# Performance work log

Measured on AMD Instinct MI355X. Metric: run time of the kernel, lower is better.

The kernel has to match this reference:

```python
import jax, jax.numpy as jnp
import numpy as np

SEQ = 4096
EMBED = 1280
HEADS = 16
HEAD_DIM = EMBED // HEADS  # 80


def rotate_half(x):
    # interleaved rotate: out[..., 2i] = -x[..., 2i+1]; out[..., 2i+1] = x[..., 2i]
    x_even = x[..., ::2]
    x_odd = x[..., 1::2]
    return jnp.stack((-x_odd, x_even), axis=-1).reshape(x.shape)


def setup_inputs() -> dict:
    key = jax.random.key(0)
    ks = jax.random.split(key, 7)
    return {
        "hidden_states": jax.random.normal(ks[0], (SEQ, EMBED), dtype=jnp.float32),
        "cos": jax.random.uniform(ks[1], (SEQ, HEAD_DIM), dtype=jnp.float32),
        "sin": jax.random.uniform(ks[2], (SEQ, HEAD_DIM), dtype=jnp.float32),
        "w_qkv": jax.random.normal(ks[3], (EMBED, 3 * EMBED), dtype=jnp.float32) * 0.02,
        "b_qkv": jax.random.normal(ks[4], (3 * EMBED,), dtype=jnp.float32) * 0.02,
        "w_proj": jax.random.normal(ks[5], (EMBED, EMBED), dtype=jnp.float32) * 0.02,
        "b_proj": jax.random.normal(ks[6], (EMBED,), dtype=jnp.float32) * 0.02,
    }


def reference(hidden_states, cos, sin, w_qkv, b_qkv, w_proj, b_proj):
    S = hidden_states.shape[0]
    # QKV projection: (S, 3E) -> (S, 3, H, D)
    qkv = (hidden_states @ w_qkv + b_qkv).reshape(S, 3, HEADS, HEAD_DIM)
    q, k, v = qkv[:, 0], qkv[:, 1], qkv[:, 2]  # each (S, H, D)

    # RoPE in float32, cos/sin broadcast over heads: (S, 1, D)
    dt = q.dtype
    qf, kf = q.astype(jnp.float32), k.astype(jnp.float32)
    c = cos[:, None, :].astype(jnp.float32)
    s = sin[:, None, :].astype(jnp.float32)
    q = (qf * c + rotate_half(qf) * s).astype(dt)
    k = (kf * c + rotate_half(kf) * s).astype(dt)

    scaling = HEAD_DIM ** -0.5
    # attention scores per head: (H, S, S)
    scores = jnp.einsum("shd,thd->hst", q, k) * scaling
    attn = jax.nn.softmax(scores.astype(jnp.float32), axis=-1).astype(dt)
    # weighted values: (S, H, D)
    out = jnp.einsum("hst,thd->shd", attn, v).reshape(S, EMBED)
    return out @ w_proj + b_proj
```

## Files before the change

### kernel.cpp

```cpp
#include <hip/hip_runtime.h>
#include <hip/hip_bf16.h>

#define SEQ   4096
#define EMBED 1280
#define NH    16
#define HD    80
#define K1    EMBED
#define N1    (3*EMBED)

typedef short bfrag_t __attribute__((ext_vector_type(8)));
typedef float f32x4   __attribute__((ext_vector_type(4)));
typedef float f32x16  __attribute__((ext_vector_type(16)));

static __device__ __forceinline__ unsigned short f2bf(float x){
    __hip_bfloat16 h = __float2bfloat16(x);
    return __builtin_bit_cast(unsigned short, h);
}
static __device__ __forceinline__ float bf2f(unsigned short u){
    unsigned int v = ((unsigned int)u) << 16;
    return __builtin_bit_cast(float, v);
}

static __device__ __forceinline__ unsigned int pack2bf(float a, float b){
    unsigned int ua = __builtin_bit_cast(unsigned int, a) + 0x8000u;
    unsigned int ub = __builtin_bit_cast(unsigned int, b) + 0x8000u;
#if __has_builtin(__builtin_amdgcn_perm)
    return __builtin_amdgcn_perm(ub, ua, 0x07060302u);
#else
    return (ua >> 16) | (ub & 0xFFFF0000u);
#endif
}

static __device__ __forceinline__ float fast_exp2(float x){
#if __has_builtin(__builtin_amdgcn_exp2f)
    return __builtin_amdgcn_exp2f(x);
#else
    return __expf(x * 0.69314718056f);
#endif
}

static __device__ __forceinline__ void gload_lds16(const void* g, void* l){
#if __has_builtin(__builtin_amdgcn_global_load_lds)
    __builtin_amdgcn_global_load_lds(
        (const __attribute__((address_space(1))) unsigned int*)g,
        (__attribute__((address_space(3))) unsigned int*)l, 16, 0, 0);
#else
    *(uint4*)l = *(const uint4*)g;
#endif
}

static __device__ __forceinline__ bfrag_t ld_frag8(const unsigned short* p){
    uint2 lo = *(const uint2*)p;
    uint2 hi = *(const uint2*)(p + 4);
    uint4 u; u.x = lo.x; u.y = lo.y; u.z = hi.x; u.w = hi.y;
    return __builtin_bit_cast(bfrag_t, u);
}

#define CONV_BLOCKS (SEQ*EMBED/4/256)
#define TQ_BX (N1/32)
#define TQ_BLOCKS (TQ_BX*(K1/32))
#define TP_BX (EMBED/32)
#define TP_BLOCKS (TP_BX*(EMBED/32))

__global__ __launch_bounds__(256)
void prep_all(const float* __restrict__ hs, unsigned short* __restrict__ hb,
              const float* __restrict__ wqkv, unsigned short* __restrict__ wqT,
              const float* __restrict__ wproj, unsigned short* __restrict__ wpT)
{
    __shared__ float t[32][33];
    int b = blockIdx.x;
    if (b < CONV_BLOCKS){
        int i = b * 256 + threadIdx.x;
        float4 v = ((const float4*)hs)[i];
        ushort4 r;
        r.x = f2bf(v.x); r.y = f2bf(v.y); r.z = f2bf(v.z); r.w = f2bf(v.w);
        ((ushort4*)hb)[i] = r;
        return;
    }
    const float* in; unsigned short* outp; int R, C, bc, br;
    if (b < CONV_BLOCKS + TQ_BLOCKS){
        b -= CONV_BLOCKS;
        in = wqkv; outp = wqT; R = K1; C = N1;
        bc = (b % TQ_BX) * 32; br = (b / TQ_BX) * 32;
    } else {
        b -= CONV_BLOCKS + TQ_BLOCKS;
        in = wproj; outp = wpT; R = EMBED; C = EMBED;
        bc = (b % TP_BX) * 32; br = (b / TP_BX) * 32;
    }
    int tx = threadIdx.x & 31, ty = threadIdx.x >> 5;
    for (int i = ty; i < 32; i += 8) t[i][tx] = in[(size_t)(br + i) * C + bc + tx];
    __syncthreads();
    for (int i = ty; i < 32; i += 8) outp[(size_t)(bc + i) * R + br + tx] = f2bf(t[tx][i]);
}


__global__ __launch_bounds__(256, 4)
void gemm_qkv(const unsigned short* __restrict__ A,
              const unsigned short* __restrict__ BT,
              const float* __restrict__ bias,
              const float* __restrict__ cosp, const float* __restrict__ sinp,
              unsigned short* __restrict__ qout, unsigned short* __restrict__ kout,
              unsigned short* __restrict__ vout,
              int M, int N, int K)
{
    __shared__ union {
        struct { unsigned short A[128*32]; unsigned short B[128*32]; } ab;
        unsigned short tr[4][64][72];
    } lds;

    int tid  = threadIdx.x;
    int lane = tid & 63, wave = tid >> 6;
    int wm = wave >> 1, wn = wave & 1;
    int quad = lane >> 4, l16 = lane & 15;
    int m0 = blockIdx.y * 128, n0 = blockIdx.x * 128;

    f32x4 acc[4][4] = {};
    const unsigned short* ga = A  + (size_t)(m0 + (tid>>2)) * K + (tid&3)*8;
    const unsigned short* gb = BT + (size_t)(n0 + (tid>>2)) * K + (tid&3)*8;

    for (int k0 = 0; k0 < K; k0 += 32){
        __syncthreads();
        gload_lds16(ga,                &lds.ab.A[tid*8]);
        gload_lds16(ga + (size_t)64*K, &lds.ab.A[2048 + tid*8]);
        gload_lds16(gb,                &lds.ab.B[tid*8]);
        gload_lds16(gb + (size_t)64*K, &lds.ab.B[2048 + tid*8]);
        ga += 32; gb += 32;
        __syncthreads();
        bfrag_t af[4], bf[4];
        #pragma unroll
        for (int i = 0; i < 4; i++)
            af[i] = *(const bfrag_t*)&lds.ab.A[(wm*64 + i*16 + l16)*32 + quad*8];
        #pragma unroll
        for (int j = 0; j < 4; j++)
            bf[j] = *(const bfrag_t*)&lds.ab.B[(wn*64 + j*16 + l16)*32 + quad*8];
        #pragma unroll
        for (int i = 0; i < 4; i++)
            #pragma unroll
            for (int j = 0; j < 4; j++)
                acc[i][j] = __builtin_amdgcn_mfma_f32_16x16x32_bf16(af[i], bf[j], acc[i][j], 0, 0, 0);
    }

    const float scaling = 0.11180339887498949f;

    if (n0 >= 2*EMBED){
        __syncthreads();
        #pragma unroll
        for (int j = 0; j < 4; j++){
            int colw = j*16 + l16;
            float b = bias[n0 + wn*64 + colw];
            #pragma unroll
            for (int i = 0; i < 4; i++){
                ushort4 u;
                u.x = f2bf(acc[i][j][0] + b);
                u.y = f2bf(acc[i][j][1] + b);
                u.z = f2bf(acc[i][j][2] + b);
                u.w = f2bf(acc[i][j][3] + b);
                *(ushort4*)&lds.tr[wave][colw][i*16 + quad*4] = u;
            }
        }
        int c8 = lane >> 3, rc = lane & 7;
        #pragma unroll
        for (int cg = 0; cg < 8; cg++){
            int colw = cg*8 + c8;
            size_t colg = (size_t)(n0 - 2*EMBED) + wn*64 + colw;
            int rowg = m0 + wm*64 + rc*8;
            *(uint4*)&vout[colg*SEQ + rowg] = *(const uint4*)&lds.tr[wave][colw][rc*8];
        }
        return;
    }

    #pragma unroll
    for (int i = 0; i < 4; i++)
    #pragma unroll
    for (int j = 0; j < 4; j++){
        int colj  = n0 + wn*64 + j*16;
        int which = colj / EMBED;
        int rem   = colj - which*EMBED;
        int hh    = rem / HD;
        int dd    = rem - hh*HD;
        float b = bias[colj + l16];
        unsigned short* dst = (which == 0) ? qout : kout;
        float mult = (which == 0) ? scaling : 1.f;
        #pragma unroll
        for (int r = 0; r < 4; r++){
            int row = m0 + wm*64 + i*16 + quad*4 + r;
            float v = acc[i][j][r] + b;
            float vo = __shfl_xor(v, 1, 64);
            float c = cosp[(size_t)row*HD + dd + l16];
            float s = sinp[(size_t)row*HD + dd + l16];
            float o = (l16 & 1) ? (v*c + vo*s) : (v*c - vo*s);
            dst[((size_t)hh*SEQ + row)*HD + dd + l16] = f2bf(o * mult);
        }
    }
}


__global__ __launch_bounds__(256, 4)
void gemm_proj(const unsigned short* __restrict__ A,
               const unsigned short* __restrict__ BT,
               const float* __restrict__ bias,
               float* __restrict__ out,
               int M, int N, int K)
{
    __shared__ unsigned short As[64*32];
    __shared__ unsigned short Bs[128*32];
    int tid  = threadIdx.x;
    int lane = tid & 63, wave = tid >> 6;
    int wm = wave & 1, wn = wave >> 1;
    int quad = lane >> 4, l16 = lane & 15;
    int m0 = blockIdx.y * 64, n0 = blockIdx.x * 128;

    f32x4 acc[2][4] = {};
    const unsigned short* ga = A  + (size_t)(m0 + (tid>>2)) * K + (tid&3)*8;
    const unsigned short* gb = BT + (size_t)(n0 + (tid>>2)) * K + (tid&3)*8;

    for (int k0 = 0; k0 < K; k0 += 32){
        __syncthreads();
        gload_lds16(ga,                &As[tid*8]);
        gload_lds16(gb,                &Bs[tid*8]);
        gload_lds16(gb + (size_t)64*K, &Bs[2048 + tid*8]);
        ga += 32; gb += 32;
        __syncthreads();
        bfrag_t af[2], bf[4];
        #pragma unroll
        for (int i = 0; i < 2; i++)
            af[i] = *(const bfrag_t*)&As[(wm*32 + i*16 + l16)*32 + quad*8];
        #pragma unroll
        for (int j = 0; j < 4; j++)
            bf[j] = *(const bfrag_t*)&Bs[(wn*64 + j*16 + l16)*32 + quad*8];
        #pragma unroll
        for (int i = 0; i < 2; i++)
            #pragma unroll
            for (int j = 0; j < 4; j++)
                acc[i][j] = __builtin_amdgcn_mfma_f32_16x16x32_bf16(af[i], bf[j], acc[i][j], 0, 0, 0);
    }

    #pragma unroll
    for (int i = 0; i < 2; i++)
    #pragma unroll
    for (int j = 0; j < 4; j++){
        int col = n0 + wn*64 + j*16 + l16;
        float b = bias[col];
        #pragma unroll
        for (int r = 0; r < 4; r++){
            int row = m0 + wm*32 + i*16 + quad*4 + r;
            out[(size_t)row * N + col] = acc[i][j][r] + b;
        }
    }
}


__global__ __launch_bounds__(256, 4)
void attn_mfma(const unsigned short* __restrict__ q,
               const unsigned short* __restrict__ k,
               const unsigned short* __restrict__ vt,
               unsigned short* __restrict__ out,
               unsigned short* __restrict__ opart,
               float* __restrict__ lpart,
               int iters)
{
    __shared__ unsigned short Vt[2][80*64];
    __shared__ unsigned short Ps[128][68];

    int tid  = threadIdx.x;
    int lane = tid & 63, wave = tid >> 6;
    int quad = lane >> 4, l16 = lane & 15;
    int l32  = lane & 31, h2 = lane >> 5;
    int h = blockIdx.y, q0 = blockIdx.x * 128;
    int split = blockIdx.z;
    int kb0 = split * iters * 64;
    int qrow = wave*32 + l32;

    const unsigned short* qh = q  + ((size_t)h*SEQ + q0)*HD;
    const unsigned short* kh = k  + (size_t)h*SEQ*HD;
    const unsigned short* vh = vt + (size_t)h*HD*SEQ;

    bfrag_t qf[5];
    #pragma unroll
    for (int kk = 0; kk < 5; kk++)
        qf[kk] = *(const bfrag_t*)&qh[(size_t)qrow*HD + (kk*2 + h2)*8];

    auto stage = [&](int buf, int kb){
        unsigned short* dst = &Vt[buf][0];
        #pragma unroll
        for (int rnd = 0; rnd < 3; rnd++){
            int idx = rnd*256 + tid;
            if (rnd < 2 || tid < 128){
                int row = idx >> 3, c = idx & 7;
                gload_lds16(&vh[(size_t)row*SEQ + kb + ((c ^ (row & 7)) << 3)], &dst[idx*8]);
            }
        }
    };

    stage(0, kb0);

    float la = 0.f, lb = 0.f;
    f32x4 o_[2][5] = {};

    const unsigned short* kp = kh + (size_t)(kb0 + l32)*HD + h2*8;
    const float LOG2E = 1.44269504f;
    const float BIAS2 = -17.3123405f;

    for (int kt = 0; kt < iters; kt++){
        f32x16 S0 = {}, S1 = {};
        #pragma unroll
        for (int kk = 0; kk < 5; kk++){
            bfrag_t kf0 = *(const bfrag_t*)(kp + kk*16);
            bfrag_t kf1 = *(const bfrag_t*)(kp + (size_t)32*HD + kk*16);
            S0 = __builtin_amdgcn_mfma_f32_32x32x16_bf16(kf0, qf[kk], S0, 0,0,0);
            S1 = __builtin_amdgcn_mfma_f32_32x32x16_bf16(kf1, qf[kk], S1, 0,0,0);
        }
        kp += (size_t)64*HD;

        #pragma unroll
        for (int r = 0; r < 16; r++){
            float p0 = fast_exp2(fmaf(S0[r], LOG2E, BIAS2));
            float p1 = fast_exp2(fmaf(S1[r], LOG2E, BIAS2));
            S0[r] = p0; S1[r] = p1;
            la += p0; lb += p1;
        }

        #pragma unroll
        for (int g = 0; g < 4; g++){
            uint2 w0, w1;
            w0.x = pack2bf(S0[g*4+0], S0[g*4+1]);
            w0.y = pack2bf(S0[g*4+2], S0[g*4+3]);
            w1.x = pack2bf(S1[g*4+0], S1[g*4+1]);
            w1.y = pack2bf(S1[g*4+2], S1[g*4+3]);
            *(uint2*)&Ps[qrow][g*8 + h2*4]      = w0;
            *(uint2*)&Ps[qrow][32 + g*8 + h2*4] = w1;
        }

        __syncthreads();
        if (kt + 1 < iters) stage((kt+1)&1, kb0 + (kt+1)*64);

        int buf = kt & 1;
        #pragma unroll
        for (int kk = 0; kk < 2; kk++){
            bfrag_t pf0 = ld_frag8(&Ps[wave*32      + l16][kk*32 + quad*8]);
            bfrag_t pf1 = ld_frag8(&Ps[wave*32 + 16 + l16][kk*32 + quad*8]);
            #pragma unroll
            for (int dt = 0; dt < 5; dt++){
                int row = dt*16 + l16;
                bfrag_t vf = *(const bfrag_t*)&Vt[buf][row*64 + (((kk*4+quad) ^ (l16 & 7)) << 3)];
                o_[0][dt] = __builtin_amdgcn_mfma_f32_16x16x32_bf16(vf, pf0, o_[0][dt], 0,0,0);
                o_[1][dt] = __builtin_amdgcn_mfma_f32_16x16x32_bf16(vf, pf1, o_[1][dt], 0,0,0);
            }
        }
    }

    float l_ = la + lb;
    l_ += __shfl_xor(l_, 32, 64);

    if (gridDim.z == 1){
        #pragma unroll
        for (int i = 0; i < 2; i++){
            float linv = 1.f / __shfl(l_, i*16 + l16, 64);
            int qg = q0 + wave*32 + i*16 + l16;
            #pragma unroll
            for (int dt = 0; dt < 5; dt++){
                int d = dt*16 + quad*4;
                ushort4 u;
                u.x = f2bf(o_[i][dt][0]*linv);
                u.y = f2bf(o_[i][dt][1]*linv);
                u.z = f2bf(o_[i][dt][2]*linv);
                u.w = f2bf(o_[i][dt][3]*linv);
                *(ushort4*)&out[(size_t)qg*EMBED + h*HD + d] = u;
            }
        }
    } else {
        if (h2 == 0)
            lpart[((size_t)(split*NH + h))*SEQ + q0 + qrow] = l_;
        #pragma unroll
        for (int i = 0; i < 2; i++){
            int qg = q0 + wave*32 + i*16 + l16;
            size_t base = (((size_t)(split*NH + h))*SEQ + qg)*HD;
            #pragma unroll
            for (int dt = 0; dt < 5; dt++){
                int d = dt*16 + quad*4;
                ushort4 u;
                u.x = f2bf(o_[i][dt][0]);
                u.y = f2bf(o_[i][dt][1]);
                u.z = f2bf(o_[i][dt][2]);
                u.w = f2bf(o_[i][dt][3]);
                *(ushort4*)&opart[base + d] = u;
            }
        }
    }
}

__global__ __launch_bounds__(256)
void attn_combine(const unsigned short* __restrict__ op,
                  const float* __restrict__ lp,
                  unsigned short* __restrict__ out,
                  int ns)
{
    int t = blockIdx.x*256 + threadIdx.x;
    int d8 = t % 10;
    int qh = t / 10;
    int q  = qh & (SEQ-1);
    int h  = qh >> 12;
    float lsum = 0.f;
    for (int s = 0; s < ns; s++) lsum += lp[((size_t)(s*NH + h))*SEQ + q];
    float inv = 1.f / lsum;
    float acc[8] = {};
    for (int s = 0; s < ns; s++){
        uint4 A = *(const uint4*)&op[(((size_t)(s*NH + h))*SEQ + q)*HD + d8*8];
        unsigned int* a = (unsigned int*)&A;
        #pragma unroll
        for (int e = 0; e < 4; e++){
            acc[2*e]   += bf2f((unsigned short)(a[e] & 0xffff));
            acc[2*e+1] += bf2f((unsigned short)(a[e] >> 16));
        }
    }
    uint4 R;
    unsigned int* r = (unsigned int*)&R;
    #pragma unroll
    for (int e = 0; e < 4; e++)
        r[e] = pack2bf(acc[2*e]*inv, acc[2*e+1]*inv);
    *(uint4*)&out[(size_t)q*EMBED + h*HD + d8*8] = R;
}


extern "C" void kernel_launch(void* const* d_in, const int* in_sizes, int n_in,
                              void* d_out, int out_size, void* d_ws, size_t ws_size,
                              hipStream_t stream)
{
    const float* hs    = (const float*)d_in[0];
    const float* cosp  = (const float*)d_in[1];
    const float* sinp  = (const float*)d_in[2];
    const float* wqkv  = (const float*)d_in[3];
    const float* bqkv  = (const float*)d_in[4];
    const float* wproj = (const float*)d_in[5];
    const float* bproj = (const float*)d_in[6];
    float* out = (float*)d_out;

    char* ws = (char*)d_ws;
    size_t off = 0;
    auto alloc = [&](size_t bytes){ void* p = ws + off; off += bytes; return p; };
    unsigned short* hb    = (unsigned short*)alloc((size_t)SEQ*EMBED*2);
    unsigned short* wqT   = (unsigned short*)alloc((size_t)N1*K1*2);
    unsigned short* wpT   = (unsigned short*)alloc((size_t)EMBED*EMBED*2);
    unsigned short* q_ws  = (unsigned short*)alloc((size_t)SEQ*EMBED*2);
    unsigned short* k_ws  = (unsigned short*)alloc((size_t)SEQ*EMBED*2);
    unsigned short* v_ws  = (unsigned short*)alloc((size_t)SEQ*EMBED*2);
    unsigned short* a_ws  = (unsigned short*)alloc((size_t)SEQ*EMBED*2);
    size_t base = off;
    size_t per_split = (size_t)NH*SEQ*HD*2 + (size_t)NH*SEQ*4;
    int nsplit = 1;
    if (ws_size >= base + 4*per_split)      nsplit = 4;
    else if (ws_size >= base + 2*per_split) nsplit = 2;
    unsigned short* opart = (unsigned short*)alloc((size_t)nsplit*NH*SEQ*HD*2);
    float*          lpart = (float*)alloc((size_t)nsplit*NH*SEQ*4);

    prep_all<<<CONV_BLOCKS + TQ_BLOCKS + TP_BLOCKS, 256, 0, stream>>>(
        hs, hb, wqkv, wqT, wproj, wpT);

    gemm_qkv<<<dim3(N1/128, SEQ/128), 256, 0, stream>>>(
        hb, wqT, bqkv, cosp, sinp, q_ws, k_ws, v_ws, SEQ, N1, K1);

    attn_mfma<<<dim3(SEQ/128, NH, nsplit), 256, 0, stream>>>(
        q_ws, k_ws, v_ws, a_ws, opart, lpart, (SEQ/64)/nsplit);
    if (nsplit > 1)
        attn_combine<<<NH*SEQ*10/256, 256, 0, stream>>>(opart, lpart, a_ws, nsplit);

    gemm_proj<<<dim3(EMBED/128, SEQ/64), 256, 0, stream>>>(
        a_ws, wpT, bproj, out, SEQ, EMBED, EMBED);
}
```

Baseline: 322.6 us.

## Split QK^T into two sequential halves, use hardware bf16 pack, cap split-K at two

```diff
diff --git a/kernel.cpp b/kernel.cpp
--- a/kernel.cpp
+++ b/kernel.cpp
@@ -22,12 +22,17 @@
 }
 
 static __device__ __forceinline__ unsigned int pack2bf(float a, float b){
+#if __has_builtin(__builtin_amdgcn_cvt_pk_bf16_f32)
+    short2 p = __builtin_amdgcn_cvt_pk_bf16_f32(a, b);
+    return __builtin_bit_cast(unsigned int, p);
+#else
     unsigned int ua = __builtin_bit_cast(unsigned int, a) + 0x8000u;
     unsigned int ub = __builtin_bit_cast(unsigned int, b) + 0x8000u;
 #if __has_builtin(__builtin_amdgcn_perm)
     return __builtin_amdgcn_perm(ub, ua, 0x07060302u);
 #else
     return (ua >> 16) | (ub & 0xFFFF0000u);
+#endif
 #endif
 }
 
@@ -302,33 +307,49 @@
     const float BIAS2 = -17.3123405f;
 
     for (int kt = 0; kt < iters; kt++){
-        f32x16 S0 = {}, S1 = {};
-        #pragma unroll
-        for (int kk = 0; kk < 5; kk++){
-            bfrag_t kf0 = *(const bfrag_t*)(kp + kk*16);
-            bfrag_t kf1 = *(const bfrag_t*)(kp + (size_t)32*HD + kk*16);
-            S0 = __builtin_amdgcn_mfma_f32_32x32x16_bf16(kf0, qf[kk], S0, 0,0,0);
-            S1 = __builtin_amdgcn_mfma_f32_32x32x16_bf16(kf1, qf[kk], S1, 0,0,0);
-        }
+        bfrag_t kf[5];
+        #pragma unroll
+        for (int kk = 0; kk < 5; kk++)
+            kf[kk] = *(const bfrag_t*)(kp + kk*16);
+        f32x16 S = {};
+        #pragma unroll
+        for (int kk = 0; kk < 5; kk++)
+            S = __builtin_amdgcn_mfma_f32_32x32x16_bf16(kf[kk], qf[kk], S, 0,0,0);
+
+        bfrag_t kg[5];
+        #pragma unroll
+        for (int kk = 0; kk < 5; kk++)
+            kg[kk] = *(const bfrag_t*)(kp + (size_t)32*HD + kk*16);
         kp += (size_t)64*HD;
 
         #pragma unroll
         for (int r = 0; r < 16; r++){
-            float p0 = fast_exp2(fmaf(S0[r], LOG2E, BIAS2));
-            float p1 = fast_exp2(fmaf(S1[r], LOG2E, BIAS2));
-            S0[r] = p0; S1[r] = p1;
-            la += p0; lb += p1;
-        }
-
+            float p = fast_exp2(fmaf(S[r], LOG2E, BIAS2));
+            S[r] = p; la += p;
+        }
         #pragma unroll
         for (int g = 0; g < 4; g++){
-            uint2 w0, w1;
-            w0.x = pack2bf(S0[g*4+0], S0[g*4+1]);
-            w0.y = pack2bf(S0[g*4+2], S0[g*4+3]);
-            w1.x = pack2bf(S1[g*4+0], S1[g*4+1]);
-            w1.y = pack2bf(S1[g*4+2], S1[g*4+3]);
-            *(uint2*)&Ps[qrow][g*8 + h2*4]      = w0;
-            *(uint2*)&Ps[qrow][32 + g*8 + h2*4] = w1;
+            uint2 w;
+            w.x = pack2bf(S[g*4+0], S[g*4+1]);
+            w.y = pack2bf(S[g*4+2], S[g*4+3]);
+            *(uint2*)&Ps[qrow][g*8 + h2*4] = w;
+        }
+
+        f32x16 T = {};
+        #pragma unroll
+        for (int kk = 0; kk < 5; kk++)
+            T = __builtin_amdgcn_mfma_f32_32x32x16_bf16(kg[kk], qf[kk], T, 0,0,0);
+        #pragma unroll
+        for (int r = 0; r < 16; r++){
+            float p = fast_exp2(fmaf(T[r], LOG2E, BIAS2));
+            T[r] = p; lb += p;
+        }
+        #pragma unroll
+        for (int g = 0; g < 4; g++){
+            uint2 w;
+            w.x = pack2bf(T[g*4+0], T[g*4+1]);
+            w.y = pack2bf(T[g*4+2], T[g*4+3]);
+            *(uint2*)&Ps[qrow][32 + g*8 + h2*4] = w;
         }
 
         __syncthreads();
@@ -447,9 +468,7 @@
     unsigned short* a_ws  = (unsigned short*)alloc((size_t)SEQ*EMBED*2);
     size_t base = off;
     size_t per_split = (size_t)NH*SEQ*HD*2 + (size_t)NH*SEQ*4;
-    int nsplit = 1;
-    if (ws_size >= base + 4*per_split)      nsplit = 4;
-    else if (ws_size >= base + 2*per_split) nsplit = 2;
+    int nsplit = (ws_size >= base + 2*per_split) ? 2 : 1;
     unsigned short* opart = (unsigned short*)alloc((size_t)nsplit*NH*SEQ*HD*2);
     float*          lpart = (float*)alloc((size_t)nsplit*NH*SEQ*4);
 
```

Result: faster. 316.1 us (-2.0%).
